# Optimization experiments

Hardware: AMD Instinct MI355X
Metric: run time of the kernel (lower is better)

## Reference

```python
import jax, jax.numpy as jnp
import numpy as np


def setup_inputs() -> dict:
    key = jax.random.key(0)
    k1, _ = jax.random.split(key)
    x = jax.random.normal(k1, (8, 128, 56, 56), dtype=jnp.float32)
    gamma = jnp.array(0.5, dtype=jnp.float32)  # learned scalar (init gamma=0.5)
    return {"x": x, "gamma": gamma}


def reference(x, gamma):
    # conv=False path: query/key/value convs are Identity, so Q=K=V=x flattened.
    B, C, H, W = x.shape
    N = H * W
    v = x.reshape(B, C, N)                          # [B, C, N]
    # energy[b, i, j] = sum_c x[b, c, i] * x[b, c, j]  (Q^T K)
    energy = jnp.einsum('bci,bcj->bij', v, v)       # [B, N, N]
    # multiplicative mask: zero out the diagonal BEFORE softmax (not -inf)
    mask = 1.0 - jnp.eye(N, dtype=energy.dtype)
    attention = jax.nn.softmax(energy * mask, axis=-1)  # [B, N, N]
    # out = bmm(V, attention): out[b, c, j] = sum_i v[b, c, i] * attention[b, i, j]
    out = jnp.einsum('bci,bij->bcj', v, attention)  # [B, C, N]
    out = jax.nn.relu(out).reshape(B, C, H, W)
    y = gamma * out + x
    return (y, out, x, gamma)
```

## Files before the change

### kernel.cpp

```cpp
#include <hip/hip_runtime.h>
#include <math.h>

#define Bb 8
#define Cc 128
#define Nn 3136
#define Np 3200
#define NT 50
#define NRT 49
#define Mm (Bb*Cc*Nn)
#define PADV 72
#define L2E 1.44269504088896340736f
#define C44 (44.0f * L2E)
#define ESCL 256.0f
#define KDEC (L2E / 256.0f)

#define XT2B (NT*16*64*8)
#define XC2B (NT*8*128*8)
#define ETILE 4096
#define EBATCH ((size_t)NRT*NRT*ETILE)
#define WS_BASE (131072 + 2*(size_t)Bb*XT2B*2)

typedef unsigned short u16;
typedef unsigned int   u32;
typedef __attribute__((ext_vector_type(8)))  u16      u16x8;
typedef __attribute__((ext_vector_type(8)))  _Float16 f16x8;
typedef __attribute__((ext_vector_type(4)))  _Float16 f16x4;
typedef __attribute__((ext_vector_type(4)))  u32      u32x4;
typedef __attribute__((ext_vector_type(4)))  float    f32x4;
typedef __attribute__((ext_vector_type(16))) float    f32x16;

__device__ __forceinline__ float exp2fast(float x) {
#if __has_builtin(__builtin_amdgcn_exp2f)
    return __builtin_amdgcn_exp2f(x);
#else
    float r; asm("v_exp_f32 %0, %1" : "=v"(r) : "v"(x)); return r;
#endif
}

typedef __attribute__((address_space(1))) const unsigned int gas_u32;
typedef __attribute__((address_space(3))) unsigned int las_u32;
__device__ __forceinline__ void gload_lds16(const u16* g, u16* l) {
    __builtin_amdgcn_global_load_lds((gas_u32*)g, (las_u32*)l, 16, 0, 0);
}

#define BAR()    __builtin_amdgcn_s_barrier()
#define SCHED0() __builtin_amdgcn_sched_barrier(0)
#define W_ALL()  asm volatile("s_waitcnt vmcnt(0) lgkmcnt(0)" ::: "memory")

__device__ __forceinline__ u32 pack_i16(float a, float b) {
    const int qa = (int)a, qb = (int)b;
    return (u32)(qa & 0xffff) | ((u32)qb << 16);
}

__global__ __launch_bounds__(256) void prep_kernel(const float* __restrict__ x,
                                                   const float* __restrict__ gamma_p,
                                                   float* __restrict__ out,
                                                   u16* __restrict__ xt2,
                                                   u16* __restrict__ xc2,
                                                   float* __restrict__ row_d) {
    const int bx = blockIdx.x;
    const int b = bx / 50, nblk = bx % 50;
    const int t = threadIdx.x;

    if (nblk == 49) {
        const u16x8 z8 = {0, 0, 0, 0, 0, 0, 0, 0};
        u16* dt = xt2 + ((size_t)b * NT + 49) * (16 * 64 * 8);
        u16* dc = xc2 + ((size_t)b * NT + 49) * (8 * 128 * 8);
        #pragma unroll
        for (int it = 0; it < 4; ++it) {
            *(u16x8*)&dt[(it * 256 + t) * 8] = z8;
            *(u16x8*)&dc[(it * 256 + t) * 8] = z8;
        }
        if (t < 64) row_d[b * Np + Nn + t] = 1.0f;
        return;
    }

    __shared__ float lx[Cc][65];
    const int n0 = nblk * 64;

    #pragma unroll 8
    for (int r = 0; r < 32; ++r) {
        const int c = r * 4 + (t >> 6);
        const int g = (b * Cc + c) * Nn + n0 + (t & 63);
        lx[c][t & 63] = x[g];
    }
    __syncthreads();

    {
        const int nl = t & 63, cseg = t >> 6;
        u16x8 hv[4];
        #pragma unroll
        for (int cc = 0; cc < 32; ++cc) {
            const _Float16 hh = (_Float16)lx[cseg * 32 + cc][nl];
            hv[cc >> 3][cc & 7] = __builtin_bit_cast(u16, hh);
        }
        u16* base = xt2 + (((size_t)(b * NT + nblk) * 16 + cseg * 4) * 64 + nl) * 8;
        #pragma unroll
        for (int k = 0; k < 4; ++k) *(u16x8*)&base[k * (64 * 8)] = hv[k];
    }
    {
        const int c = t >> 1, half = t & 1;
        u16x8 hv[4];
        #pragma unroll
        for (int k = 0; k < 32; ++k) {
            const _Float16 hh = (_Float16)lx[c][half * 32 + k];
            hv[k >> 3][k & 7] = __builtin_bit_cast(u16, hh);
        }
        u16* base = xc2 + (((size_t)(b * NT + nblk) * 8 + half * 4) * 128 + c) * 8;
        #pragma unroll
        for (int k = 0; k < 4; ++k) *(u16x8*)&base[k * (128 * 8)] = hv[k];
    }
    if (bx == 0 && t == 0) out[(size_t)3 * Mm] = gamma_p[0];
}

__global__ __launch_bounds__(256, 4) void e_kernel(const u16* __restrict__ xt2,
                                                   u16* __restrict__ E,
                                                   float* __restrict__ row_d,
                                                   int bofs, int nb) {
    const int bx = blockIdx.x;
    const int b_ = bx % nb, rem = bx / nb;
    const int jt = rem >> 2, iq = rem & 3;
    const int b = bofs + b_;
    const int t = threadIdx.x;
    const int w = t >> 6, l = t & 63, lane = l & 31, h = l >> 5;
    const int isub = w & 1, jgrp = w >> 1;
    const u16* __restrict__ xb = xt2 + (size_t)b * XT2B;

    f16x8 Bj[8];
    const int jrow = jgrp * 32 + lane;
    #pragma unroll
    for (int kk = 0; kk < 8; ++kk)
        Bj[kk] = *(const f16x8*)&xb[(((size_t)jt * 16 + 2 * kk + h) * 64 + jrow) * 8];

    const int it0 = iq * 12 + (iq ? 1 : 0);
    const int icnt = iq ? 12 : 13;
    const int arow = isub * 32 + lane;

    float dA = 0.f, dB = 0.f;
    for (int it = it0; it < it0 + icnt; ++it) {
        const u16* ab = &xb[((size_t)it * 16 * 64 + arow) * 8];
        f32x16 ea;
        #pragma unroll
        for (int r = 0; r < 16; ++r) ea[r] = 0.f;
        __builtin_amdgcn_s_setprio(1);
        #pragma unroll
        for (int kk = 0; kk < 8; ++kk) {
            const f16x8 A = *(const f16x8*)&ab[(2 * kk + h) * 512];
            ea = __builtin_amdgcn_mfma_f32_32x32x16_f16(A, Bj[kk], ea, 0, 0, 0);
        }
        __builtin_amdgcn_s_setprio(0);

        const bool dt = (it == jt) && (isub == jgrp);
        u32 pk[4][2], sw[4][2];
        #pragma unroll
        for (int qq = 0; qq < 4; ++qq) {
            float pv[4];
            #pragma unroll
            for (int r2 = 0; r2 < 4; ++r2) {
                const int m = qq * 8 + h * 4 + r2;
                float v = ea[qq * 4 + r2];
                if (dt && m == lane) v = 0.f;
                pv[r2] = v;
                const float e = exp2fast(fmaf(v, L2E, -C44));
                if (r2 & 1) dB += e; else dA += e;
            }
            pk[qq][0] = pack_i16(pv[0] * ESCL, pv[1] * ESCL);
            pk[qq][1] = pack_i16(pv[2] * ESCL, pv[3] * ESCL);
            sw[qq][0] = __shfl_xor(pk[qq][0], 32, 64);
            sw[qq][1] = __shfl_xor(pk[qq][1], 32, 64);
        }
        u16* eb = E + ((((size_t)(b_ * NRT + jt) * NRT + it) * 2 + jgrp) * 4) * 512;
        #pragma unroll
        for (int kt = 0; kt < 2; ++kt) {
            u32x4 bw;
            bw[0] = h ? sw[2 * kt + 1][0] : pk[2 * kt][0];
            bw[1] = h ? sw[2 * kt + 1][1] : pk[2 * kt][1];
            bw[2] = h ? pk[2 * kt + 1][0] : sw[2 * kt][0];
            bw[3] = h ? pk[2 * kt + 1][1] : sw[2 * kt][1];
            *(u32x4*)&eb[(isub * 2 + kt) * 512 + l * 8] = bw;
        }
    }
    float d = dA + dB;
    d += __shfl_xor(d, 32, 64);
    if (h == 0) atomicAdd(&row_d[b * Np + jt * 64 + jgrp * 32 + lane], d);
}

__global__ __launch_bounds__(256) void conv_kernel(float* __restrict__ row_d) {
    const int i = blockIdx.x * 256 + threadIdx.x;
    row_d[i] = C44 + __log2f(row_d[i]);
}

__global__ __launch_bounds__(256, 3) void pv_kernel(const u16* __restrict__ xc2,
                                                    const u16* __restrict__ E,
                                                    const float* __restrict__ row_c,
                                                    float* __restrict__ out,
                                                    int bofs, int nb) {
    __shared__ __align__(16) u16 s_e[2][ETILE];

    const int bx = blockIdx.x;
    const int b_ = bx % nb, rem = bx / nb;
    const int jt = rem >> 1, kh = rem & 1;
    const int b = bofs + b_;
    const int it0 = kh ? 25 : 0, it1 = kh ? 49 : 25;
    const int t = threadIdx.x;
    const int w = t >> 6, l = t & 63, lane = l & 31, h = l >> 5;
    const int jg = w & 1, cp = w >> 1;
    const u16* __restrict__ xcb = xc2 + (size_t)b * XC2B;
    const u16* __restrict__ Eb = E + (size_t)(b_ * NRT + jt) * NRT * ETILE;

    f32x16 a0, a1;
    #pragma unroll
    for (int r = 0; r < 16; ++r) { a0[r] = 0.f; a1[r] = 0.f; }

    {
        const u16* gs = Eb + (size_t)it0 * ETILE + (w * 2) * 512 + l * 8;
        u16* ls = &s_e[0][(w * 2) * 512];
        gload_lds16(gs, ls);
        gload_lds16(gs + 512, ls + 512);
    }
    W_ALL(); BAR(); SCHED0();

    for (int it = it0; it < it1; ++it) {
        const int cur = (it - it0) & 1;
        if (it + 1 < it1) {
            const u16* gs = Eb + (size_t)(it + 1) * ETILE + (w * 2) * 512 + l * 8;
            u16* ls = &s_e[cur ^ 1][(w * 2) * 512];
            gload_lds16(gs, ls);
            gload_lds16(gs + 512, ls + 512);
        }

        const float* cb = &row_c[b * Np + it * 64];
        f16x8 Bp[4];
        #pragma unroll
        for (int s = 0; s < 4; ++s) {
            const u16x8 ev = *(const u16x8*)&s_e[cur][(jg * 4 + s) * 512 + l * 8];
            const f32x4 cA = *(const f32x4*)&cb[s * 16 + h * 8];
            const f32x4 cB = *(const f32x4*)&cb[s * 16 + h * 8 + 4];
            float p[8];
            #pragma unroll
            for (int e = 0; e < 8; ++e) {
                const float f = (float)(short)ev[e];
                const float c = (e < 4) ? cA[e] : cB[e - 4];
                p[e] = exp2fast(fmaf(f, KDEC, -c));
            }
            u32x4 bw;
            bw[0] = __builtin_bit_cast(u32, __builtin_amdgcn_cvt_pkrtz(p[0], p[1]));
            bw[1] = __builtin_bit_cast(u32, __builtin_amdgcn_cvt_pkrtz(p[2], p[3]));
            bw[2] = __builtin_bit_cast(u32, __builtin_amdgcn_cvt_pkrtz(p[4], p[5]));
            bw[3] = __builtin_bit_cast(u32, __builtin_amdgcn_cvt_pkrtz(p[6], p[7]));
            Bp[s] = __builtin_bit_cast(f16x8, bw);
        }

        __builtin_amdgcn_s_setprio(1);
        #pragma unroll
        for (int s = 0; s < 4; ++s) {
            const f16x8 Av0 = *(const f16x8*)&xcb[((size_t)(it * 8 + s * 2 + h) * 128 + cp * 64 + lane) * 8];
            const f16x8 Av1 = *(const f16x8*)&xcb[((size_t)(it * 8 + s * 2 + h) * 128 + cp * 64 + 32 + lane) * 8];
            a0 = __builtin_amdgcn_mfma_f32_32x32x16_f16(Av0, Bp[s], a0, 0, 0, 0);
            a1 = __builtin_amdgcn_mfma_f32_32x32x16_f16(Av1, Bp[s], a1, 0, 0, 0);
        }
        __builtin_amdgcn_s_setprio(0);

        W_ALL(); BAR(); SCHED0();
    }

    #pragma unroll
    for (int r = 0; r < 16; ++r) {
        const int mrow = (r & 3) + 8 * (r >> 2) + 4 * h;
        const int jj = jt * 64 + jg * 32 + lane;
        const size_t p0 = (size_t)(b * Cc + cp * 64 + mrow) * Nn + jj;
        const size_t p1 = (size_t)(b * Cc + cp * 64 + 32 + mrow) * Nn + jj;
        out[(size_t)kh * Mm + p0] = a0[r];
        out[(size_t)kh * Mm + p1] = a1[r];
    }
}

__global__ __launch_bounds__(256) void finish_kernel(const float* __restrict__ x,
                                                     const float* __restrict__ gamma_p,
                                                     float* __restrict__ out) {
    const float gamma = gamma_p[0];
    const size_t base = ((size_t)blockIdx.x * 256 + threadIdx.x) * 4;
    const f32x4 pa = *(const f32x4*)&out[base];
    const f32x4 pb = *(const f32x4*)&out[(size_t)Mm + base];
    const f32x4 xv = *(const f32x4*)&x[base];
    f32x4 yo, oo;
    #pragma unroll
    for (int r = 0; r < 4; ++r) {
        const float o = fmaxf(pa[r] + pb[r], 0.0f);
        oo[r] = o;
        yo[r] = fmaf(gamma, o, xv[r]);
    }
    *(f32x4*)&out[base] = yo;
    *(f32x4*)&out[(size_t)Mm + base] = oo;
    *(f32x4*)&out[(size_t)2 * Mm + base] = xv;
}

__global__ __launch_bounds__(256, 5) void stats_legacy(const u16* __restrict__ xt2,
                                                       float* __restrict__ row_d) {
    const int bx = blockIdx.x;
    const int b = bx & 7, rem = bx >> 3;
    const int i0t = rem >> 3, jq = rem & 7;
    const int t = threadIdx.x;
    const int w = t >> 6, l = t & 63, lane = l & 31, h = l >> 5;
    const int igrp = w & 1, jsub = w >> 1;
    const u16* __restrict__ xb = xt2 + (size_t)b * XT2B;

    f16x8 Bf[8];
    const int irow = igrp * 32 + lane;
    #pragma unroll
    for (int kk = 0; kk < 8; ++kk)
        Bf[kk] = *(const f16x8*)&xb[(((size_t)i0t * 16 + 2 * kk + h) * 64 + irow) * 8];

    const int jt0 = jq * 6 + (jq < 2 ? jq : 2);
    const int jcnt = 6 + (jq < 2 ? 1 : 0);
    const int jrow = jsub * 32 + lane;

    float sa = 0.f, sb = 0.f;
    for (int jt = jt0; jt < jt0 + jcnt; ++jt) {
        const u16* ab = &xb[((size_t)jt * 16 * 64 + jrow) * 8];
        f32x16 ea, eb;
        #pragma unroll
        for (int r = 0; r < 16; ++r) { ea[r] = 0.f; eb[r] = 0.f; }
        #pragma unroll
        for (int kk = 0; kk < 4; ++kk) {
            const f16x8 A0 = *(const f16x8*)&ab[(4 * kk + h) * 512];
            const f16x8 A1 = *(const f16x8*)&ab[(4 * kk + 2 + h) * 512];
            ea = __builtin_amdgcn_mfma_f32_32x32x16_f16(A0, Bf[2 * kk],     ea, 0, 0, 0);
            eb = __builtin_amdgcn_mfma_f32_32x32x16_f16(A1, Bf[2 * kk + 1], eb, 0, 0, 0);
        }
        const bool diag = (jt == i0t) && (jsub == igrp);
        #pragma unroll
        for (int r = 0; r < 16; ++r) {
            const int mrow = (r & 3) + 8 * (r >> 2) + 4 * h;
            float v = ea[r] + eb[r];
            if (diag && mrow == lane) v = 0.f;
            const float e = exp2fast(fmaf(v, L2E, -C44));
            if (r & 1) sb += e; else sa += e;
        }
    }
    float ssum = sa + sb;
    ssum += __shfl_xor(ssum, 32, 64);
    if (h == 0) atomicAdd(&row_d[b * Np + i0t * 64 + igrp * 32 + lane], ssum);
}

__global__ __launch_bounds__(256, 3) void out_legacy(const u16* __restrict__ xt2,
                                                     const u16* __restrict__ xc2,
                                                     const float* __restrict__ row_c,
                                                     float* __restrict__ out) {
    __shared__ u16 s_pt[2][64 * PADV];

    const int bx = blockIdx.x;
    const int b = bx & 7, rem = bx >> 3;
    const int j0t = rem >> 1, ih = rem & 1;
    const int ti0 = ih * 25, ti1 = ti0 + 25;
    const int t = threadIdx.x;
    const int w = t >> 6, l = t & 63, lane = l & 31, h = l >> 5;
    const int isub = w & 1, jgrp = w >> 1;
    const int jg = w & 1,  cp = w >> 1;
    const u16* __restrict__ xtb = xt2 + (size_t)b * XT2B;
    const u16* __restrict__ xcb = xc2 + (size_t)b * XC2B;

    f16x8 Bj[8];
    const int jrow = jgrp * 32 + lane;
    #pragma unroll
    for (int kk = 0; kk < 8; ++kk)
        Bj[kk] = *(const f16x8*)&xtb[(((size_t)j0t * 16 + 2 * kk + h) * 64 + jrow) * 8];

    f32x16 oa, ob;
    #pragma unroll
    for (int r = 0; r < 16; ++r) { oa[r] = 0.f; ob[r] = 0.f; }

    const int arow = isub * 32 + lane;
    const int ptbase = (jgrp * 32 + lane) * PADV + isub * 32;
    const int pbrow = (jg * 32 + lane) * PADV + h * 8;

    f16x8 Ac[8];
    {
        const u16* ab = &xtb[((size_t)ti0 * 16 * 64 + arow) * 8];
        #pragma unroll
        for (int kk = 0; kk < 8; ++kk)
            Ac[kk] = *(const f16x8*)&ab[(2 * kk + h) * 512];
    }

    for (int ti = ti0; ti < ti1; ++ti) {
        const int tn = (ti + 1 < ti1) ? ti + 1 : ti;
        f16x8 An[8];
        const u16* abn = &xtb[((size_t)tn * 16 * 64 + arow) * 8];
        #pragma unroll
        for (int kk = 0; kk < 8; ++kk)
            An[kk] = *(const f16x8*)&abn[(2 * kk + h) * 512];

        f32x16 ea;
        #pragma unroll
        for (int r = 0; r < 16; ++r) ea[r] = 0.f;
        #pragma unroll
        for (int kk = 0; kk < 8; ++kk)
            ea = __builtin_amdgcn_mfma_f32_32x32x16_f16(Ac[kk], Bj[kk], ea, 0, 0, 0);

        u16* pt = &s_pt[ti & 1][0];
        const float* cbase = &row_c[b * Np + ti * 64 + isub * 32];
        const bool dsub = (ti == j0t) && (isub == jgrp);
        #pragma unroll
        for (int qq = 0; qq < 4; ++qq) {
            const f32x4 cv = *(const f32x4*)&cbase[qq * 8 + h * 4];
            f16x4 pv;
            #pragma unroll
            for (int r = 0; r < 4; ++r) {
                const int m = qq * 8 + h * 4 + r;
                float v = ea[qq * 4 + r];
                if (dsub && m == lane) v = 0.f;
                pv[r] = (_Float16)exp2fast(fmaf(v, L2E, -cv[r]));
            }
            *(f16x4*)&pt[ptbase + qq * 8 + h * 4] = pv;
        }

        f16x8 Av[4][2];
        const u16* vb = &xcb[((size_t)ti * 8 * 128 + cp * 64 + lane) * 8];
        #pragma unroll
        for (int kk = 0; kk < 4; ++kk) {
            Av[kk][0] = *(const f16x8*)&vb[((2 * kk + h) * 128) * 8];
            Av[kk][1] = *(const f16x8*)&vb[((2 * kk + h) * 128 + 32) * 8];
        }
        __syncthreads();

        #pragma unroll
        for (int kk = 0; kk < 4; ++kk) {
            const f16x8 Bp = *(const f16x8*)&pt[pbrow + kk * 16];
            oa = __builtin_amdgcn_mfma_f32_32x32x16_f16(Av[kk][0], Bp, oa, 0, 0, 0);
            ob = __builtin_amdgcn_mfma_f32_32x32x16_f16(Av[kk][1], Bp, ob, 0, 0, 0);
        }
        #pragma unroll
        for (int kk = 0; kk < 8; ++kk) Ac[kk] = An[kk];
    }

    #pragma unroll
    for (int r = 0; r < 16; ++r) {
        const int mrow = (r & 3) + 8 * (r >> 2) + 4 * h;
        const int jj = j0t * 64 + jg * 32 + lane;
        const size_t p0 = (size_t)(b * Cc + cp * 64 + mrow) * Nn + jj;
        const size_t p1 = (size_t)(b * Cc + cp * 64 + 32 + mrow) * Nn + jj;
        out[(size_t)ih * Mm + p0] = oa[r];
        out[(size_t)ih * Mm + p1] = ob[r];
    }
}

extern "C" void kernel_launch(void* const* d_in, const int* in_sizes, int n_in,
                              void* d_out, int out_size, void* d_ws, size_t ws_size,
                              hipStream_t stream) {
    const float* x       = (const float*)d_in[0];
    const float* gamma_p = (const float*)d_in[1];
    float* out = (float*)d_out;

    float* row_d = (float*)d_ws;
    u16* xt2 = (u16*)((char*)d_ws + (1 << 17));
    u16* xc2 = xt2 + (size_t)Bb * XT2B;
    u16* E   = (u16*)((char*)d_ws + WS_BASE);
    const size_t ebytes1 = EBATCH * 2;

    hipMemsetAsync(row_d, 0, (size_t)Bb * Np * sizeof(float), stream);
    prep_kernel<<<400, 256, 0, stream>>>(x, gamma_p, out, xt2, xc2, row_d);

    int nb = 0;
    if      (ws_size >= WS_BASE + 8 * ebytes1) nb = 8;
    else if (ws_size >= WS_BASE + 4 * ebytes1) nb = 4;
    else if (ws_size >= WS_BASE + 2 * ebytes1) nb = 2;

    if (nb) {
        for (int bofs = 0; bofs < Bb; bofs += nb) {
            e_kernel <<<nb * 196, 256, 0, stream>>>(xt2, E, row_d, bofs, nb);
            conv_kernel<<<(nb * Np) / 256, 256, 0, stream>>>(row_d + (size_t)bofs * Np);
            pv_kernel<<<nb * 98, 256, 0, stream>>>(xc2, E, row_d, out, bofs, nb);
        }
    } else {
        stats_legacy<<<3136, 256, 0, stream>>>(xt2, row_d);
        conv_kernel <<<100, 256, 0, stream>>>(row_d);
        out_legacy  <<<784, 256, 0, stream>>>(xt2, xc2, row_d, out);
    }
    finish_kernel<<<3136, 256, 0, stream>>>(x, gamma_p, out);
}
```

Baseline: 198.3 us.

## Triple-buffer PV E-tile loads, split K three ways, dual accumulators in QK

The PV kernel now splits the key range into three partitions instead of two, which gives more blocks, and writes three partial outputs that the finish kernel sums. Its LDS staging changes from double to triple buffering with a partial vmcnt wait, so tile loads run two iterations ahead and only the oldest one is waited on. The E kernel splits its MFMA chain into two independent accumulators to shorten the dependency chain. The cost is more LDS per block, an extra partial-output buffer to write and read back in finish, and a memset on the legacy path.

```diff
diff --git a/kernel.cpp b/kernel.cpp
--- a/kernel.cpp
+++ b/kernel.cpp
@@ -46,6 +46,7 @@
 #define BAR()    __builtin_amdgcn_s_barrier()
 #define SCHED0() __builtin_amdgcn_sched_barrier(0)
 #define W_ALL()  asm volatile("s_waitcnt vmcnt(0) lgkmcnt(0)" ::: "memory")
+#define W_VM2()  asm volatile("s_waitcnt vmcnt(2)" ::: "memory")
 
 __device__ __forceinline__ u32 pack_i16(float a, float b) {
     const int qa = (int)a, qb = (int)b;
@@ -139,14 +140,16 @@
     float dA = 0.f, dB = 0.f;
     for (int it = it0; it < it0 + icnt; ++it) {
         const u16* ab = &xb[((size_t)it * 16 * 64 + arow) * 8];
-        f32x16 ea;
-        #pragma unroll
-        for (int r = 0; r < 16; ++r) ea[r] = 0.f;
+        f32x16 ea, eb;
+        #pragma unroll
+        for (int r = 0; r < 16; ++r) { ea[r] = 0.f; eb[r] = 0.f; }
         __builtin_amdgcn_s_setprio(1);
         #pragma unroll
-        for (int kk = 0; kk < 8; ++kk) {
-            const f16x8 A = *(const f16x8*)&ab[(2 * kk + h) * 512];
-            ea = __builtin_amdgcn_mfma_f32_32x32x16_f16(A, Bj[kk], ea, 0, 0, 0);
+        for (int kk = 0; kk < 4; ++kk) {
+            const f16x8 A0 = *(const f16x8*)&ab[(4 * kk + h) * 512];
+            const f16x8 A1 = *(const f16x8*)&ab[(4 * kk + 2 + h) * 512];
+            ea = __builtin_amdgcn_mfma_f32_32x32x16_f16(A0, Bj[2 * kk],     ea, 0, 0, 0);
+            eb = __builtin_amdgcn_mfma_f32_32x32x16_f16(A1, Bj[2 * kk + 1], eb, 0, 0, 0);
         }
         __builtin_amdgcn_s_setprio(0);
 
@@ -158,7 +161,7 @@
             #pragma unroll
             for (int r2 = 0; r2 < 4; ++r2) {
                 const int m = qq * 8 + h * 4 + r2;
-                float v = ea[qq * 4 + r2];
+                float v = ea[qq * 4 + r2] + eb[qq * 4 + r2];
                 if (dt && m == lane) v = 0.f;
                 pv[r2] = v;
                 const float e = exp2fast(fmaf(v, L2E, -C44));
@@ -169,7 +172,7 @@
             sw[qq][0] = __shfl_xor(pk[qq][0], 32, 64);
             sw[qq][1] = __shfl_xor(pk[qq][1], 32, 64);
         }
-        u16* eb = E + ((((size_t)(b_ * NRT + jt) * NRT + it) * 2 + jgrp) * 4) * 512;
+        u16* eb2 = E + ((((size_t)(b_ * NRT + jt) * NRT + it) * 2 + jgrp) * 4) * 512;
         #pragma unroll
         for (int kt = 0; kt < 2; ++kt) {
             u32x4 bw;
@@ -177,7 +180,7 @@
             bw[1] = h ? sw[2 * kt + 1][1] : pk[2 * kt][1];
             bw[2] = h ? pk[2 * kt + 1][0] : sw[2 * kt][0];
             bw[3] = h ? pk[2 * kt + 1][1] : sw[2 * kt][1];
-            *(u32x4*)&eb[(isub * 2 + kt) * 512 + l * 8] = bw;
+            *(u32x4*)&eb2[(isub * 2 + kt) * 512 + l * 8] = bw;
         }
     }
     float d = dA + dB;
@@ -195,13 +198,14 @@
                                                     const float* __restrict__ row_c,
                                                     float* __restrict__ out,
                                                     int bofs, int nb) {
-    __shared__ __align__(16) u16 s_e[2][ETILE];
+    __shared__ __align__(16) u16 s_e[3][ETILE];
 
     const int bx = blockIdx.x;
     const int b_ = bx % nb, rem = bx / nb;
-    const int jt = rem >> 1, kh = rem & 1;
+    const int jt = rem / 3, kq = rem % 3;
     const int b = bofs + b_;
-    const int it0 = kh ? 25 : 0, it1 = kh ? 49 : 25;
+    const int it0 = (kq == 0) ? 0 : (kq == 1 ? 17 : 33);
+    const int it1 = (kq == 0) ? 17 : (kq == 1 ? 33 : 49);
     const int t = threadIdx.x;
     const int w = t >> 6, l = t & 63, lane = l & 31, h = l >> 5;
     const int jg = w & 1, cp = w >> 1;
@@ -218,16 +222,16 @@
         gload_lds16(gs, ls);
         gload_lds16(gs + 512, ls + 512);
     }
-    W_ALL(); BAR(); SCHED0();
+    {
+        const u16* gs = Eb + (size_t)(it0 + 1) * ETILE + (w * 2) * 512 + l * 8;
+        u16* ls = &s_e[1][(w * 2) * 512];
+        gload_lds16(gs, ls);
+        gload_lds16(gs + 512, ls + 512);
+    }
+    W_VM2(); BAR(); SCHED0();
 
     for (int it = it0; it < it1; ++it) {
-        const int cur = (it - it0) & 1;
-        if (it + 1 < it1) {
-            const u16* gs = Eb + (size_t)(it + 1) * ETILE + (w * 2) * 512 + l * 8;
-            u16* ls = &s_e[cur ^ 1][(w * 2) * 512];
-            gload_lds16(gs, ls);
-            gload_lds16(gs + 512, ls + 512);
-        }
+        const int cur = (it - it0) % 3;
 
         const float* cb = &row_c[b * Np + it * 64];
         f16x8 Bp[4];
@@ -260,8 +264,15 @@
             a1 = __builtin_amdgcn_mfma_f32_32x32x16_f16(Av1, Bp[s], a1, 0, 0, 0);
         }
         __builtin_amdgcn_s_setprio(0);
-
-        W_ALL(); BAR(); SCHED0();
+        SCHED0();
+
+        if (it + 2 < it1) {
+            const u16* gs = Eb + (size_t)(it + 2) * ETILE + (w * 2) * 512 + l * 8;
+            u16* ls = &s_e[(it + 2 - it0) % 3][(w * 2) * 512];
+            gload_lds16(gs, ls);
+            gload_lds16(gs + 512, ls + 512);
+        }
+        W_VM2(); BAR(); SCHED0();
     }
 
     #pragma unroll
@@ -270,8 +281,8 @@
         const int jj = jt * 64 + jg * 32 + lane;
         const size_t p0 = (size_t)(b * Cc + cp * 64 + mrow) * Nn + jj;
         const size_t p1 = (size_t)(b * Cc + cp * 64 + 32 + mrow) * Nn + jj;
-        out[(size_t)kh * Mm + p0] = a0[r];
-        out[(size_t)kh * Mm + p1] = a1[r];
+        out[(size_t)kq * Mm + p0] = a0[r];
+        out[(size_t)kq * Mm + p1] = a1[r];
     }
 }
 
@@ -282,11 +293,12 @@
     const size_t base = ((size_t)blockIdx.x * 256 + threadIdx.x) * 4;
     const f32x4 pa = *(const f32x4*)&out[base];
     const f32x4 pb = *(const f32x4*)&out[(size_t)Mm + base];
+    const f32x4 pc = *(const f32x4*)&out[(size_t)2 * Mm + base];
     const f32x4 xv = *(const f32x4*)&x[base];
     f32x4 yo, oo;
     #pragma unroll
     for (int r = 0; r < 4; ++r) {
-        const float o = fmaxf(pa[r] + pb[r], 0.0f);
+        const float o = fmaxf(pa[r] + pb[r] + pc[r], 0.0f);
         oo[r] = o;
         yo[r] = fmaf(gamma, o, xv[r]);
     }
@@ -469,9 +481,10 @@
         for (int bofs = 0; bofs < Bb; bofs += nb) {
             e_kernel <<<nb * 196, 256, 0, stream>>>(xt2, E, row_d, bofs, nb);
             conv_kernel<<<(nb * Np) / 256, 256, 0, stream>>>(row_d + (size_t)bofs * Np);
-            pv_kernel<<<nb * 98, 256, 0, stream>>>(xc2, E, row_d, out, bofs, nb);
+            pv_kernel<<<nb * 147, 256, 0, stream>>>(xc2, E, row_d, out, bofs, nb);
         }
     } else {
+        hipMemsetAsync(out + (size_t)2 * Mm, 0, (size_t)Mm * sizeof(float), stream);
         stats_legacy<<<3136, 256, 0, stream>>>(xt2, row_d);
         conv_kernel <<<100, 256, 0, stream>>>(row_d);
         out_legacy  <<<784, 256, 0, stream>>>(xt2, xc2, row_d, out);
```

Result: slower. 207.3 us (+4.6%).
